# Kernel optimization log

Measured on AMD Instinct MI355X. Metric: run time of the kernel, lower is better.

Reference implementation:

```python
import jax, jax.numpy as jnp
import numpy as np

N_NODES = 100000
N_EDGES = 1000000
D_IN = 128
D_OUT = 128
ALPHA = 0.5


def setup_inputs() -> dict:
    key = jax.random.key(0)
    k = jax.random.split(key, 8)
    x = jax.random.normal(k[0], (N_NODES, D_IN), dtype=jnp.float32)
    edge_src = jax.random.randint(k[1], (N_EDGES,), 0, N_NODES, dtype=jnp.int32)
    edge_dst = jax.random.randint(k[2], (N_EDGES,), 0, N_NODES, dtype=jnp.int32)
    s = 1.0 / np.sqrt(D_IN)
    W_sd = jax.random.uniform(k[3], (D_OUT, D_IN), jnp.float32, -s, s)
    b_sd = jax.random.uniform(k[4], (D_OUT,), jnp.float32, -s, s)
    W_ds = jax.random.uniform(k[5], (D_OUT, D_IN), jnp.float32, -s, s)
    b_ds = jax.random.uniform(k[6], (D_OUT,), jnp.float32, -s, s)
    return {"x": x, "edge_src": edge_src, "edge_dst": edge_dst,
            "W_sd": W_sd, "b_sd": b_sd, "W_ds": W_ds, "b_ds": b_ds}


def reference(x, edge_src, edge_dst, W_sd, b_sd, W_ds, b_ds):
    # adj[dst, src] = 1 for each edge.
    # adj @ x      : aggregate source features into destination rows.
    # adj.T @ x    : aggregate destination features into source rows.
    agg_sd = jax.ops.segment_sum(x[edge_src], edge_dst, num_segments=N_NODES)  # [N, D_IN]
    agg_ds = jax.ops.segment_sum(x[edge_dst], edge_src, num_segments=N_NODES)  # [N, D_IN]
    src_to_dst = agg_sd @ W_sd.T + b_sd  # torch Linear: x W^T + b
    dst_to_src = agg_ds @ W_ds.T + b_ds
    return ALPHA * src_to_dst + (1.0 - ALPHA) * dst_to_src
```

## Files before the change

kernel.cpp:

```cpp
#include <hip/hip_runtime.h>

#define NN 100000
#define NE 1000000
#define D 128
#define ALPHA 0.5f

#define OFF_W2     102400000UL
#define OFF_BIAS   102531072UL
#define OFF_CNT    102531584UL
#define OFF_START  102931584UL
#define OFF_BINC   103331584UL
#define OFF_BINB   103333632UL
#define OFF_BINCUR 103335680UL
#define OFF_BUF    103337728UL
#define OFF_REC    111337728UL

#define NB  391
#define EPB 2048

__global__ __launch_bounds__(256) void build_w2b(const float* __restrict__ Wsd,
                                                 const float* __restrict__ Wds,
                                                 const float* __restrict__ bsd,
                                                 const float* __restrict__ bds,
                                                 float* __restrict__ W2,
                                                 float* __restrict__ bias) {
    int idx = blockIdx.x * 256 + threadIdx.x;
    int k = idx >> 7;
    int j = idx & 127;
    float v;
    if (k < 128) v = ALPHA * Wsd[j * D + k];
    else         v = (1.0f - ALPHA) * Wds[j * D + (k - 128)];
    W2[idx] = v;
    if (idx < 128) bias[idx] = ALPHA * bsd[idx] + (1.0f - ALPHA) * bds[idx];
}

__global__ __launch_bounds__(512) void zero_bins(int* __restrict__ binCnt) {
    int i = threadIdx.x;
    if (i < NB) binCnt[i] = 0;
}

__global__ __launch_bounds__(256) void count_bins(const int* __restrict__ esrc,
                                                  const int* __restrict__ edst,
                                                  int* __restrict__ binCnt) {
    __shared__ int h[NB];
    int t = threadIdx.x;
    for (int i = t; i < NB; i += 256) h[i] = 0;
    __syncthreads();
    int e0 = blockIdx.x * EPB;
    for (int i = t; i < EPB; i += 256) {
        int e = e0 + i;
        if (e < NE) {
            atomicAdd(&h[edst[e] >> 8], 1);
            atomicAdd(&h[esrc[e] >> 8], 1);
        }
    }
    __syncthreads();
    for (int i = t; i < NB; i += 256)
        if (h[i]) atomicAdd(&binCnt[i], h[i]);
}

__global__ __launch_bounds__(256) void scan_bins(const int* __restrict__ binCnt,
                                                 int* __restrict__ binBase,
                                                 int* __restrict__ binCursor) {
    __shared__ int v[NB];
    int t = threadIdx.x;
    for (int i = t; i < NB; i += 256) v[i] = binCnt[i];
    __syncthreads();
    if (t == 0) {
        int acc = 0;
        for (int i = 0; i < NB; ++i) { int c = v[i]; v[i] = acc; acc += c; }
    }
    __syncthreads();
    for (int i = t; i < NB; i += 256) { binBase[i] = v[i]; binCursor[i] = v[i]; }
}

__global__ __launch_bounds__(256) void place_bins(const int* __restrict__ esrc,
                                                  const int* __restrict__ edst,
                                                  int* __restrict__ binCursor,
                                                  int* __restrict__ rec4) {
    __shared__ int h[NB];
    __shared__ int base[NB];
    __shared__ int lcur[NB];
    int t = threadIdx.x;
    for (int i = t; i < NB; i += 256) h[i] = 0;
    __syncthreads();
    int e0 = blockIdx.x * EPB;
    for (int i = t; i < EPB; i += 256) {
        int e = e0 + i;
        if (e < NE) {
            atomicAdd(&h[edst[e] >> 8], 1);
            atomicAdd(&h[esrc[e] >> 8], 1);
        }
    }
    __syncthreads();
    for (int i = t; i < NB; i += 256) {
        if (h[i]) base[i] = atomicAdd(&binCursor[i], h[i]);
        lcur[i] = 0;
    }
    __syncthreads();
    for (int i = t; i < EPB; i += 256) {
        int e = e0 + i;
        if (e < NE) {
            int s = esrc[e], d = edst[e];
            int bd = d >> 8, bs = s >> 8;
            int p1 = atomicAdd(&lcur[bd], 1);
            rec4[base[bd] + p1] = ((d & 255) << 18) | (s << 1);
            int p2 = atomicAdd(&lcur[bs], 1);
            rec4[base[bs] + p2] = ((s & 255) << 18) | (d << 1) | 1;
        }
    }
}

__global__ __launch_bounds__(256) void build_csr(const int* __restrict__ rec4,
                                                 const int* __restrict__ binBase,
                                                 const int* __restrict__ binCnt,
                                                 int* __restrict__ buf,
                                                 int* __restrict__ start,
                                                 int* __restrict__ cnt_out) {
    __shared__ int hc[256];
    __shared__ int st[256];
    int b = blockIdx.x;
    int t = threadIdx.x;
    int node0 = b << 8;
    int r0 = binBase[b];
    int rn = binCnt[b];

    hc[t] = 0;
    __syncthreads();
    for (int i = t; i < rn; i += 256)
        atomicAdd(&hc[rec4[r0 + i] >> 18], 1);
    __syncthreads();
    if (t == 0) {
        int acc = 0;
        for (int i = 0; i < 256; ++i) { st[i] = acc; acc += hc[i]; }
    }
    __syncthreads();
    int n = node0 + t;
    if (n < NN) {
        start[n]   = r0 + st[t];
        cnt_out[n] = hc[t];
    }
    hc[t] = st[t];
    __syncthreads();
    for (int i = t; i < rn; i += 256) {
        int r = rec4[r0 + i];
        int pos = atomicAdd(&hc[r >> 18], 1);
        buf[r0 + pos] = r & 0x3FFFF;
    }
}

__global__ __launch_bounds__(256) void gather_z(const int* __restrict__ start,
                                                const int* __restrict__ cnt,
                                                const int* __restrict__ buf,
                                                const float* __restrict__ x,
                                                float* __restrict__ z) {
    int wave = blockIdx.x * 4 + (threadIdx.x >> 6);
    int lane = threadIdx.x & 63;
    int g    = lane >> 5;
    int gl   = lane & 31;
    int node = wave * 2 + g;
    if (node >= NN) return;
    const int s0 = start[node];
    const int e0 = s0 + cnt[node];
    const int c4 = gl << 2;

    float4 A = make_float4(0.f, 0.f, 0.f, 0.f);
    float4 B = make_float4(0.f, 0.f, 0.f, 0.f);

#define ACCUM(v, p) if ((v) & 1) { B.x += (p).x; B.y += (p).y; B.z += (p).z; B.w += (p).w; } \
                    else         { A.x += (p).x; A.y += (p).y; A.z += (p).z; A.w += (p).w; }

    int i = s0;
    for (; i + 4 <= e0; i += 4) {
        int v0 = buf[i], v1 = buf[i + 1], v2 = buf[i + 2], v3 = buf[i + 3];
        float4 p0 = *(const float4*)&x[(size_t)(v0 >> 1) * D + c4];
        float4 p1 = *(const float4*)&x[(size_t)(v1 >> 1) * D + c4];
        float4 p2 = *(const float4*)&x[(size_t)(v2 >> 1) * D + c4];
        float4 p3 = *(const float4*)&x[(size_t)(v3 >> 1) * D + c4];
        ACCUM(v0, p0) ACCUM(v1, p1) ACCUM(v2, p2) ACCUM(v3, p3)
    }
    for (; i < e0; ++i) {
        int v0 = buf[i];
        float4 p0 = *(const float4*)&x[(size_t)(v0 >> 1) * D + c4];
        ACCUM(v0, p0)
    }
#undef ACCUM

    *(float4*)&z[(size_t)node * 256 + c4]       = A;
    *(float4*)&z[(size_t)node * 256 + 128 + c4] = B;
}

__global__ __launch_bounds__(256) void transform_z(const float* __restrict__ z,
                                                   const float* __restrict__ W2,
                                                   const float* __restrict__ bias,
                                                   float* __restrict__ out) {
    __shared__ float As[64][132];
    const int tid  = threadIdx.x;
    const int brow = blockIdx.x * 64;
    const int bcol = blockIdx.y * 64;
    const int ty   = tid >> 4;
    const int tx   = tid & 15;

    float acc[4][4];
#pragma unroll
    for (int i = 0; i < 4; ++i)
#pragma unroll
        for (int j = 0; j < 4; ++j) acc[i][j] = 0.f;

    for (int kp = 0; kp < 2; ++kp) {
#pragma unroll
        for (int i = 0; i < 8; ++i) {
            int f   = tid + i * 256;
            int row = f >> 5;
            int kc  = (f & 31) << 2;
            float4 g = make_float4(0.f, 0.f, 0.f, 0.f);
            int grow = brow + row;
            if (grow < NN) g = *(const float4*)&z[(size_t)grow * 256 + kp * 128 + kc];
            *(float4*)&As[row][kc] = g;
        }
        __syncthreads();

#pragma unroll 2
        for (int k0 = 0; k0 < 128; k0 += 4) {
            float av[4][4], bv[4][4];
#pragma unroll
            for (int i = 0; i < 4; ++i) {
                float4 t = *(const float4*)&As[ty * 4 + i][k0];
                av[i][0] = t.x; av[i][1] = t.y; av[i][2] = t.z; av[i][3] = t.w;
            }
#pragma unroll
            for (int j = 0; j < 4; ++j) {
                float4 t = *(const float4*)&W2[(size_t)(kp * 128 + k0 + j) * 128 + bcol + tx * 4];
                bv[j][0] = t.x; bv[j][1] = t.y; bv[j][2] = t.z; bv[j][3] = t.w;
            }
#pragma unroll
            for (int i = 0; i < 4; ++i)
#pragma unroll
                for (int c = 0; c < 4; ++c)
#pragma unroll
                    for (int kk = 0; kk < 4; ++kk)
                        acc[i][c] += av[i][kk] * bv[kk][c];
        }
        __syncthreads();
    }

    float4 bb = *(const float4*)&bias[bcol + tx * 4];
#pragma unroll
    for (int i = 0; i < 4; ++i) {
        int row = brow + ty * 4 + i;
        if (row < NN) {
            float4 v = make_float4(acc[i][0] + bb.x, acc[i][1] + bb.y,
                                   acc[i][2] + bb.z, acc[i][3] + bb.w);
            *(float4*)&out[(size_t)row * D + bcol + tx * 4] = v;
        }
    }
}

extern "C" void kernel_launch(void* const* d_in, const int* in_sizes, int n_in,
                              void* d_out, int out_size, void* d_ws, size_t ws_size,
                              hipStream_t stream) {
    const float* x    = (const float*)d_in[0];
    const int*   esrc = (const int*)  d_in[1];
    const int*   edst = (const int*)  d_in[2];
    const float* Wsd  = (const float*)d_in[3];
    const float* bsd  = (const float*)d_in[4];
    const float* Wds  = (const float*)d_in[5];
    const float* bds  = (const float*)d_in[6];
    float* out = (float*)d_out;

    char*  ws       = (char*)d_ws;
    float* z        = (float*)ws;
    float* W2       = (float*)(ws + OFF_W2);
    float* bias     = (float*)(ws + OFF_BIAS);
    int*   cnt      = (int*)(ws + OFF_CNT);
    int*   start    = (int*)(ws + OFF_START);
    int*   binCnt   = (int*)(ws + OFF_BINC);
    int*   binBase  = (int*)(ws + OFF_BINB);
    int*   binCursor= (int*)(ws + OFF_BINCUR);
    int*   buf      = (int*)(ws + OFF_BUF);
    int*   rec4     = (int*)(ws + OFF_REC);

    const int nblk = (NE + EPB - 1) / EPB;

    build_w2b<<<128, 256, 0, stream>>>(Wsd, Wds, bsd, bds, W2, bias);
    zero_bins<<<1, 512, 0, stream>>>(binCnt);
    count_bins<<<nblk, 256, 0, stream>>>(esrc, edst, binCnt);
    scan_bins<<<1, 256, 0, stream>>>(binCnt, binBase, binCursor);
    place_bins<<<nblk, 256, 0, stream>>>(esrc, edst, binCursor, rec4);
    build_csr<<<NB, 256, 0, stream>>>(rec4, binBase, binCnt, buf, start, cnt);
    gather_z<<<12500, 256, 0, stream>>>(start, cnt, buf, x, z);
    transform_z<<<dim3((NN + 63) / 64, 2), 256, 0, stream>>>(z, W2, bias, out);
}
```

Baseline: 432.1 us.

## Stage bin records in LDS and sort each node's neighbor list in CSR build

The CSR build kernel now copies each bin's records into shared memory, scatters them into a shared-memory staging array, and insertion-sorts each node's neighbor list before writing it out with coalesced stores. This replaces repeated global reads and random global scatter writes with LDS traffic. Sorted neighbor indices should also make the later gather of x rows more cache-friendly. It costs 48KB of LDS per block, which lowers occupancy, and adds a per-thread serial sort. Bins larger than the buffer fall back to the old path.

```diff
diff --git a/kernel.cpp b/kernel.cpp
--- a/kernel.cpp
+++ b/kernel.cpp
@@ -17,6 +17,7 @@
 
 #define NB  391
 #define EPB 2048
+#define MAXBIN 6144
 
 __global__ __launch_bounds__(256) void build_w2b(const float* __restrict__ Wsd,
                                                  const float* __restrict__ Wds,
@@ -117,35 +118,70 @@
                                                  int* __restrict__ buf,
                                                  int* __restrict__ start,
                                                  int* __restrict__ cnt_out) {
+    __shared__ int recs[MAXBIN];
+    __shared__ int sorted[MAXBIN];
     __shared__ int hc[256];
+    __shared__ int cn[256];
     __shared__ int st[256];
     int b = blockIdx.x;
     int t = threadIdx.x;
     int node0 = b << 8;
     int r0 = binBase[b];
     int rn = binCnt[b];
-
+    bool fits = (rn <= MAXBIN);
+
+    if (fits)
+        for (int i = t; i < rn; i += 256) recs[i] = rec4[r0 + i];
     hc[t] = 0;
     __syncthreads();
-    for (int i = t; i < rn; i += 256)
-        atomicAdd(&hc[rec4[r0 + i] >> 18], 1);
+
+    if (fits) {
+        for (int i = t; i < rn; i += 256)
+            atomicAdd(&hc[recs[i] >> 18], 1);
+    } else {
+        for (int i = t; i < rn; i += 256)
+            atomicAdd(&hc[rec4[r0 + i] >> 18], 1);
+    }
     __syncthreads();
     if (t == 0) {
         int acc = 0;
         for (int i = 0; i < 256; ++i) { st[i] = acc; acc += hc[i]; }
     }
     __syncthreads();
+
     int n = node0 + t;
     if (n < NN) {
         start[n]   = r0 + st[t];
         cnt_out[n] = hc[t];
     }
+    cn[t] = hc[t];
     hc[t] = st[t];
     __syncthreads();
-    for (int i = t; i < rn; i += 256) {
-        int r = rec4[r0 + i];
-        int pos = atomicAdd(&hc[r >> 18], 1);
-        buf[r0 + pos] = r & 0x3FFFF;
+
+    if (fits) {
+        for (int i = t; i < rn; i += 256) {
+            int r = recs[i];
+            int pos = atomicAdd(&hc[r >> 18], 1);
+            sorted[pos] = r & 0x3FFFF;
+        }
+        __syncthreads();
+        {
+            int lo = st[t], hi = st[t] + cn[t];
+            for (int j = lo + 1; j < hi; ++j) {
+                int key = sorted[j];
+                int k = j - 1;
+                while (k >= lo && sorted[k] > key) { sorted[k + 1] = sorted[k]; --k; }
+                sorted[k + 1] = key;
+            }
+        }
+        __syncthreads();
+        for (int i = t; i < rn; i += 256) buf[r0 + i] = sorted[i];
+    } else {
+        for (int i = t; i < rn; i += 256) {
+            int r = rec4[r0 + i];
+            int pos = atomicAdd(&hc[r >> 18], 1);
+            buf[r0 + pos] = r & 0x3FFFF;
+        }
     }
 }
 
```

Result: slower. 475.0 us (+9.9%).
